# Optimization experiments

Measured on AMD Instinct MI355X. Metric: run time of the kernel, lower is better.

## Reference

```python
import jax, jax.numpy as jnp
import numpy as np

RATE = 22050.0 / 256.0  # audio_target_rate from the torch source
SIZES = [2.23147392 * RATE, 2.62519274 * RATE, 3.74199546 * RATE,
         5.78800454 * RATE, 8.02371882 * RATE, float('inf')]
WEIGHT = 1.0
EPS = 1e-7


def _giou_1d(a, b):
    # a, b: [P, 2] intervals (start, end); elementwise 1-D GIoU
    inter = jnp.clip(jnp.minimum(a[:, 1], b[:, 1]) - jnp.maximum(a[:, 0], b[:, 0]), 0.0)
    union = (a[:, 1] - a[:, 0]) + (b[:, 1] - b[:, 0]) - inter
    iou = inter / (union + EPS)
    enclose = jnp.maximum(a[:, 1], b[:, 1]) - jnp.minimum(a[:, 0], b[:, 0])
    return iou - (enclose - union) / (enclose + EPS)


def setup_inputs() -> dict:
    key = jax.random.key(0)
    ks = jax.random.split(key, 4)
    B, N = 4, 32
    L0 = 131072  # frames at the finest level
    levels = 6
    anchors = {f"anchors_l{i}": (jnp.arange(L0 >> i, dtype=jnp.float32) + 0.5) * (2.0 ** i)
               for i in range(levels)}
    A = sum(int(v.shape[0]) for v in anchors.values())  # 258048
    # GT intervals: all rows belong to class 0 (matches class_id filter in the source)
    starts = jax.random.uniform(ks[0], (B, N), minval=0.0, maxval=float(L0) - 2000.0)
    lens = jax.random.uniform(ks[1], (B, N), minval=50.0, maxval=1500.0)
    annotations = jnp.stack([starts, starts + lens, jnp.zeros((B, N))], axis=-1).astype(jnp.float32)
    # Predicted intervals for every anchor
    c = jax.random.uniform(ks[2], (B, A), minval=0.0, maxval=float(L0))
    w = jax.random.uniform(ks[3], (B, A), minval=10.0, maxval=2000.0)
    regressions = jnp.stack([c - 0.5 * w, c + 0.5 * w], axis=-1).astype(jnp.float32)
    out = {"regressions": regressions, "annotations": annotations, "class_id": 0}
    out.update(anchors)
    return out


def reference(regressions, annotations, anchors_l0, anchors_l1, anchors_l2,
              anchors_l3, anchors_l4, anchors_l5, class_id):
    anchors_list = [anchors_l0, anchors_l1, anchors_l2, anchors_l3, anchors_l4, anchors_l5]
    all_pts = jnp.concatenate(anchors_list)  # [A]

    def per_sample(reg, ann):
        # ann: [N, 3]; inputs guarantee every row has class == class_id and is valid
        order = jnp.argsort(ann[:, 1] - ann[:, 0])  # sort GT by length ascending
        ann = ann[order]
        s, e = ann[:, 0:1], ann[:, 1:2]  # [N,1]
        pos_parts, nl_parts, nr_parts = [], [], []
        for i, pts in enumerate(anchors_list):
            l = pts[None, :] - s            # [N, A_i]
            r = e - pts[None, :]            # [N, A_i]
            in_gt = (l >= 0.0) & (r >= 0.0)
            m = jnp.maximum(l, r)
            lower = SIZES[i - 1] if i > 0 else 0.0
            cand = in_gt & (m >= lower) & (m < SIZES[i])
            pos_parts.append(cand.any(axis=0))
            amax = jnp.argmax(cand, axis=0)  # first True per anchor (0 if none)
            inv = 1.0 / (2.0 ** i)           # normalize l*/r* by 2**level
            nl_parts.append(jnp.take_along_axis(l, amax[None, :], axis=0)[0] * inv)
            nr_parts.append(jnp.take_along_axis(r, amax[None, :], axis=0)[0] * inv)
        pos = jnp.concatenate(pos_parts)   # [A] bool
        nl = jnp.concatenate(nl_parts)     # [A]
        nr = jnp.concatenate(nr_parts)     # [A]
        # decoded normalized target boxes around the anchor points
        boxes = jnp.stack([all_pts - nl, all_pts + nr], axis=1)  # [A, 2]
        giou = jnp.clip(_giou_1d(boxes, reg[:, :2]), -1.0, 1.0)
        loss = 1.0 - giou
        posf = pos.astype(loss.dtype)
        # masked mean over positive anchors (torch indexes by boolean mask then .mean())
        return jnp.sum(loss * posf) / jnp.maximum(jnp.sum(posf), 1.0) * WEIGHT

    return jax.vmap(per_sample)(regressions, annotations)  # [B] per-sample losses
```

## Files before the change

kernel.cpp:

```cpp
#include <hip/hip_runtime.h>

#define EPS_F 1e-7f
#define NN 32
#define MARGIN 3

__global__ __launch_bounds__(256) void rl_sparse(
    const float* __restrict__ reg,
    const float* __restrict__ ann,
    int c0, int A,
    float* __restrict__ ws)
{
    const int n = blockIdx.x;
    const int b = blockIdx.y;
    const int t = threadIdx.x;

    __shared__ float2 sh_se[NN];

    const float sz[7] = {
        0.0f,
        (float)(2.23147392 * (22050.0 / 256.0)),
        (float)(2.62519274 * (22050.0 / 256.0)),
        (float)(3.74199546 * (22050.0 / 256.0)),
        (float)(5.78800454 * (22050.0 / 256.0)),
        (float)(8.02371882 * (22050.0 / 256.0)),
        __builtin_inff()
    };

    if (t < NN) {
        const float* an = ann + (size_t)b * (size_t)NN * 3;
        const float s0 = an[t * 3 + 0];
        const float e0 = an[t * 3 + 1];
        const float len = e0 - s0;
        int rank = 0;
#pragma unroll
        for (int j = 0; j < NN; ++j) {
            const float lj = __shfl(len, j, 64);
            rank += (lj < len) || (lj == len && j < t);
        }
        sh_se[rank] = make_float2(s0, e0);
    }
    __syncthreads();

    const float s = sh_se[n].x;
    const float e = sh_se[n].y;
    const float mid   = 0.5f * (s + e);
    const float halfL = 0.5f * (e - s);

    const int twoc0 = 2 * c0;
    float loss_sum = 0.0f, pos_sum = 0.0f;

    for (int lvl = 0; lvl < 6; ++lvl) {
        const float lo = sz[lvl];
        const float hi = sz[lvl + 1];
        const int   cnt  = c0 >> lvl;
        const int   aoff = twoc0 - (twoc0 >> lvl);
        const float scale = __int_as_float((127 + lvl) << 23);
        const float inv   = __int_as_float((127 - lvl) << 23);

        const float dlo = fmaxf(lo - halfL, 0.0f);
        const float dhi = hi - halfL;
        const float prl = fmaxf(mid + dlo, s);
        const float prh = fminf(mid + dhi, e);
        const float pll = fmaxf(mid - dhi, s);
        const float plh = fminf(mid - dlo, e);

        int r0 = (int)floorf(prl * inv - 0.5f) - MARGIN;
        int r1 = (int)floorf(prh * inv - 0.5f) + MARGIN;
        int l0 = (int)floorf(pll * inv - 0.5f) - MARGIN;
        int l1 = (int)floorf(plh * inv - 0.5f) + MARGIN;
        r0 = max(r0, 0); r1 = min(r1, cnt - 1);
        l0 = max(l0, 0); l1 = min(l1, cnt - 1);
        if (r1 >= r0) l1 = min(l1, r0 - 1);
        const int lenL = max(l1 - l0 + 1, 0);
        const int lenR = max(r1 - r0 + 1, 0);
        const int total = lenL + lenR;

        for (int j = t; j < total; j += 256) {
            const int loc = (j < lenL) ? (l0 + j) : (r0 + (j - lenL));
            const float pt = ((float)loc + 0.5f) * scale;
            const float l = pt - s;
            const float r = e - pt;
            const float m = fmaxf(l, r);
            if (!((fminf(l, r) >= 0.0f) & (m >= lo) & (m < hi))) continue;
            bool first = true;
            for (int n2 = 0; n2 < n; ++n2) {
                const float2 o = sh_se[n2];
                const float l2 = pt - o.x;
                const float r2 = o.y - pt;
                const float m2 = fmaxf(l2, r2);
                if ((fminf(l2, r2) >= 0.0f) & (m2 >= lo) & (m2 < hi)) {
                    first = false; break;
                }
            }
            if (!first) continue;
            const float b0 = pt - l * inv;
            const float b1 = pt + r * inv;
            const float2 g = ((const float2*)reg)[(size_t)b * A + (aoff + loc)];
            const float inter = fmaxf(fminf(b1, g.y) - fmaxf(b0, g.x), 0.0f);
            const float uni = (b1 - b0) + (g.y - g.x) - inter;
            const float iou = inter * __builtin_amdgcn_rcpf(uni + EPS_F);
            const float enc = fmaxf(b1, g.y) - fminf(b0, g.x);
            float giou = iou - (enc - uni) * __builtin_amdgcn_rcpf(enc + EPS_F);
            giou = fminf(fmaxf(giou, -1.0f), 1.0f);
            loss_sum += 1.0f - giou;
            pos_sum  += 1.0f;
        }
    }

    for (int o = 32; o > 0; o >>= 1) {
        loss_sum += __shfl_down(loss_sum, o, 64);
        pos_sum  += __shfl_down(pos_sum,  o, 64);
    }
    __shared__ float red_l[4], red_p[4];
    const int wave = t >> 6;
    if ((t & 63) == 0) { red_l[wave] = loss_sum; red_p[wave] = pos_sum; }
    __syncthreads();
    if (t == 0) {
        float Ls = red_l[0] + red_l[1] + red_l[2] + red_l[3];
        float Ps = red_p[0] + red_p[1] + red_p[2] + red_p[3];
        float* slot = ws + ((size_t)b * NN + n) * 2;
        slot[0] = Ls;
        slot[1] = Ps;
    }
}

__global__ void rl_fin(const float* __restrict__ ws, float* __restrict__ out,
                       int gx) {
    const int b = threadIdx.x >> 6;
    const int lane = threadIdx.x & 63;
    float Ls = 0.0f, Ps = 0.0f;
    for (int i = lane; i < gx; i += 64) {
        const float2 p = *(const float2*)(ws + ((size_t)b * gx + i) * 2);
        Ls += p.x;
        Ps += p.y;
    }
    for (int o = 32; o > 0; o >>= 1) {
        Ls += __shfl_down(Ls, o, 64);
        Ps += __shfl_down(Ps, o, 64);
    }
    if (lane == 0) out[b] = Ls / fmaxf(Ps, 1.0f);
}

extern "C" void kernel_launch(void* const* d_in, const int* in_sizes, int n_in,
                              void* d_out, int out_size, void* d_ws, size_t ws_size,
                              hipStream_t stream) {
    const float* reg = (const float*)d_in[0];
    const float* ann = (const float*)d_in[1];
    const int c0 = in_sizes[3];
    const int A = in_sizes[3] + in_sizes[4] + in_sizes[5] +
                  in_sizes[6] + in_sizes[7] + in_sizes[8];
    const int B = out_size;

    float* ws = (float*)d_ws;
    dim3 grid(NN, B);
    rl_sparse<<<grid, 256, 0, stream>>>(reg, ann, c0, A, ws);
    rl_fin<<<1, 64 * B, 0, stream>>>(ws, (float*)d_out, NN);
}
```

Measured before the change: 79.94 us.

## Fuse sparse loss and final reduction into one kernel per sample

The two-kernel scheme (one block per GT per sample plus a finalize kernel) is replaced by one block per sample, where each wave loops over GT intervals with stride 4 and the block reduces straight to the output. This removes the second launch and the workspace round trip. In exchange only B blocks (4) run on a GPU with many CUs, and each wave processes its anchor ranges serially in 64-lane strides, so total latency may grow substantially.

```diff
diff --git a/kernel.cpp b/kernel.cpp
--- a/kernel.cpp
+++ b/kernel.cpp
@@ -4,15 +4,16 @@
 #define NN 32
 #define MARGIN 3
 
-__global__ __launch_bounds__(256) void rl_sparse(
+__global__ __launch_bounds__(256) void rl_fused(
     const float* __restrict__ reg,
     const float* __restrict__ ann,
     int c0, int A,
-    float* __restrict__ ws)
+    float* __restrict__ out)
 {
-    const int n = blockIdx.x;
-    const int b = blockIdx.y;
+    const int b = blockIdx.x;
     const int t = threadIdx.x;
+    const int wave = t >> 6;
+    const int lane = t & 63;
 
     __shared__ float2 sh_se[NN];
 
@@ -41,69 +42,71 @@
     }
     __syncthreads();
 
-    const float s = sh_se[n].x;
-    const float e = sh_se[n].y;
-    const float mid   = 0.5f * (s + e);
-    const float halfL = 0.5f * (e - s);
-
     const int twoc0 = 2 * c0;
     float loss_sum = 0.0f, pos_sum = 0.0f;
 
-    for (int lvl = 0; lvl < 6; ++lvl) {
-        const float lo = sz[lvl];
-        const float hi = sz[lvl + 1];
-        const int   cnt  = c0 >> lvl;
-        const int   aoff = twoc0 - (twoc0 >> lvl);
-        const float scale = __int_as_float((127 + lvl) << 23);
-        const float inv   = __int_as_float((127 - lvl) << 23);
+    for (int n = wave; n < NN; n += 4) {
+        const float s = sh_se[n].x;
+        const float e = sh_se[n].y;
+        const float mid   = 0.5f * (s + e);
+        const float halfL = 0.5f * (e - s);
 
-        const float dlo = fmaxf(lo - halfL, 0.0f);
-        const float dhi = hi - halfL;
-        const float prl = fmaxf(mid + dlo, s);
-        const float prh = fminf(mid + dhi, e);
-        const float pll = fmaxf(mid - dhi, s);
-        const float plh = fminf(mid - dlo, e);
+        for (int lvl = 0; lvl < 6; ++lvl) {
+            const float lo = sz[lvl];
+            const float hi = sz[lvl + 1];
+            const int   cnt  = c0 >> lvl;
+            const int   aoff = twoc0 - (twoc0 >> lvl);
+            const float scale = __int_as_float((127 + lvl) << 23);
+            const float inv   = __int_as_float((127 - lvl) << 23);
 
-        int r0 = (int)floorf(prl * inv - 0.5f) - MARGIN;
-        int r1 = (int)floorf(prh * inv - 0.5f) + MARGIN;
-        int l0 = (int)floorf(pll * inv - 0.5f) - MARGIN;
-        int l1 = (int)floorf(plh * inv - 0.5f) + MARGIN;
-        r0 = max(r0, 0); r1 = min(r1, cnt - 1);
-        l0 = max(l0, 0); l1 = min(l1, cnt - 1);
-        if (r1 >= r0) l1 = min(l1, r0 - 1);
-        const int lenL = max(l1 - l0 + 1, 0);
-        const int lenR = max(r1 - r0 + 1, 0);
-        const int total = lenL + lenR;
+            const float dlo = fmaxf(lo - halfL, 0.0f);
+            const float dhi = hi - halfL;
+            const float prl = fmaxf(mid + dlo, s);
+            const float prh = fminf(mid + dhi, e);
+            const float pll = fmaxf(mid - dhi, s);
+            const float plh = fminf(mid - dlo, e);
 
-        for (int j = t; j < total; j += 256) {
-            const int loc = (j < lenL) ? (l0 + j) : (r0 + (j - lenL));
-            const float pt = ((float)loc + 0.5f) * scale;
-            const float l = pt - s;
-            const float r = e - pt;
-            const float m = fmaxf(l, r);
-            if (!((fminf(l, r) >= 0.0f) & (m >= lo) & (m < hi))) continue;
-            bool first = true;
-            for (int n2 = 0; n2 < n; ++n2) {
-                const float2 o = sh_se[n2];
-                const float l2 = pt - o.x;
-                const float r2 = o.y - pt;
-                const float m2 = fmaxf(l2, r2);
-                if ((fminf(l2, r2) >= 0.0f) & (m2 >= lo) & (m2 < hi)) {
-                    first = false; break;
+            int r0 = (int)floorf(prl * inv - 0.5f) - MARGIN;
+            int r1 = (int)floorf(prh * inv - 0.5f) + MARGIN;
+            int l0 = (int)floorf(pll * inv - 0.5f) - MARGIN;
+            int l1 = (int)floorf(plh * inv - 0.5f) + MARGIN;
+            r0 = max(r0, 0); r1 = min(r1, cnt - 1);
+            l0 = max(l0, 0); l1 = min(l1, cnt - 1);
+            if (r1 >= r0) l1 = min(l1, r0 - 1);
+            const int lenL = max(l1 - l0 + 1, 0);
+            const int lenR = max(r1 - r0 + 1, 0);
+            const int total = lenL + lenR;
+
+            for (int j = lane; j < total; j += 64) {
+                const int loc = (j < lenL) ? (l0 + j) : (r0 + (j - lenL));
+                const float pt = ((float)loc + 0.5f) * scale;
+                const float l = pt - s;
+                const float r = e - pt;
+                const float m = fmaxf(l, r);
+                if (!((fminf(l, r) >= 0.0f) & (m >= lo) & (m < hi))) continue;
+                bool first = true;
+                for (int n2 = 0; n2 < n; ++n2) {
+                    const float2 o = sh_se[n2];
+                    const float l2 = pt - o.x;
+                    const float r2 = o.y - pt;
+                    const float m2 = fmaxf(l2, r2);
+                    if ((fminf(l2, r2) >= 0.0f) & (m2 >= lo) & (m2 < hi)) {
+                        first = false; break;
+                    }
                 }
+                if (!first) continue;
+                const float b0 = pt - l * inv;
+                const float b1 = pt + r * inv;
+                const float2 g = ((const float2*)reg)[(size_t)b * A + (aoff + loc)];
+                const float inter = fmaxf(fminf(b1, g.y) - fmaxf(b0, g.x), 0.0f);
+                const float uni = (b1 - b0) + (g.y - g.x) - inter;
+                const float iou = inter * __builtin_amdgcn_rcpf(uni + EPS_F);
+                const float enc = fmaxf(b1, g.y) - fminf(b0, g.x);
+                float giou = iou - (enc - uni) * __builtin_amdgcn_rcpf(enc + EPS_F);
+                giou = fminf(fmaxf(giou, -1.0f), 1.0f);
+                loss_sum += 1.0f - giou;
+                pos_sum  += 1.0f;
             }
-            if (!first) continue;
-            const float b0 = pt - l * inv;
-            const float b1 = pt + r * inv;
-            const float2 g = ((const float2*)reg)[(size_t)b * A + (aoff + loc)];
-            const float inter = fmaxf(fminf(b1, g.y) - fmaxf(b0, g.x), 0.0f);
-            const float uni = (b1 - b0) + (g.y - g.x) - inter;
-            const float iou = inter * __builtin_amdgcn_rcpf(uni + EPS_F);
-            const float enc = fmaxf(b1, g.y) - fminf(b0, g.x);
-            float giou = iou - (enc - uni) * __builtin_amdgcn_rcpf(enc + EPS_F);
-            giou = fminf(fmaxf(giou, -1.0f), 1.0f);
-            loss_sum += 1.0f - giou;
-            pos_sum  += 1.0f;
         }
     }
 
@@ -112,33 +115,13 @@
         pos_sum  += __shfl_down(pos_sum,  o, 64);
     }
     __shared__ float red_l[4], red_p[4];
-    const int wave = t >> 6;
-    if ((t & 63) == 0) { red_l[wave] = loss_sum; red_p[wave] = pos_sum; }
+    if (lane == 0) { red_l[wave] = loss_sum; red_p[wave] = pos_sum; }
     __syncthreads();
     if (t == 0) {
-        float Ls = red_l[0] + red_l[1] + red_l[2] + red_l[3];
-        float Ps = red_p[0] + red_p[1] + red_p[2] + red_p[3];
-        float* slot = ws + ((size_t)b * NN + n) * 2;
-        slot[0] = Ls;
-        slot[1] = Ps;
+        const float Ls = red_l[0] + red_l[1] + red_l[2] + red_l[3];
+        const float Ps = red_p[0] + red_p[1] + red_p[2] + red_p[3];
+        out[b] = Ls / fmaxf(Ps, 1.0f);
     }
-}
-
-__global__ void rl_fin(const float* __restrict__ ws, float* __restrict__ out,
-                       int gx) {
-    const int b = threadIdx.x >> 6;
-    const int lane = threadIdx.x & 63;
-    float Ls = 0.0f, Ps = 0.0f;
-    for (int i = lane; i < gx; i += 64) {
-        const float2 p = *(const float2*)(ws + ((size_t)b * gx + i) * 2);
-        Ls += p.x;
-        Ps += p.y;
-    }
-    for (int o = 32; o > 0; o >>= 1) {
-        Ls += __shfl_down(Ls, o, 64);
-        Ps += __shfl_down(Ps, o, 64);
-    }
-    if (lane == 0) out[b] = Ls / fmaxf(Ps, 1.0f);
 }
 
 extern "C" void kernel_launch(void* const* d_in, const int* in_sizes, int n_in,
@@ -151,8 +134,5 @@
                   in_sizes[6] + in_sizes[7] + in_sizes[8];
     const int B = out_size;
 
-    float* ws = (float*)d_ws;
-    dim3 grid(NN, B);
-    rl_sparse<<<grid, 256, 0, stream>>>(reg, ann, c0, A, ws);
-    rl_fin<<<1, 64 * B, 0, stream>>>(ws, (float*)d_out, NN);
+    rl_fused<<<dim3(B), 256, 0, stream>>>(reg, ann, c0, A, (float*)d_out);
 }
```

After: 126.1 us. 57.8% more time.
